# Performance work log

Measured on AMD Instinct MI355X. Metric: run time of the kernel, lower is better.

The kernel has to match this reference:

```python
import jax, jax.numpy as jnp
import numpy as np

EPS = 1e-12  # matches torch F.normalize default eps


def _l2norm(x):
    n = jnp.linalg.norm(x, axis=-1, keepdims=True)
    return x / jnp.maximum(n, EPS)


def setup_inputs() -> dict:
    key = jax.random.key(0)
    k1, k2 = jax.random.split(key)
    B, Na, T, Nv, D = 16, 128, 10, 196, 256
    audio_feats = jax.random.normal(k1, (B, Na, D), dtype=jnp.float32)
    visual_feats = jax.random.normal(k2, (B, T, Nv, D), dtype=jnp.float32)
    temperature = jnp.asarray(2.0, dtype=jnp.float32)
    return {"audio_feats": audio_feats, "visual_feats": visual_feats,
            "temperature": temperature}


def reference(audio_feats, visual_feats, temperature):
    # audio_feats: (B, Na, D); visual_feats: (B, T, Nv, D)
    a = _l2norm(audio_feats)                         # (B, Na, D)
    v = _l2norm(visual_feats)                        # (B, T, Nv, D)
    # all-pairs token-level cosine sims: (Bx, By, Na, T, Nv)
    sims = jnp.einsum('xad,ytvd->xyatv', a, v) / temperature
    # aggregate: max over patches, mean over time, mean over audio tokens
    clip_sims = sims.max(axis=-1).mean(axis=-1).mean(axis=-1)  # (B, B)

    # InfoNCE on diagonal
    B = clip_sims.shape[0]
    diag = jnp.arange(B)
    log_p_a2v = jax.nn.log_softmax(clip_sims, axis=1)
    log_p_v2a = jax.nn.log_softmax(clip_sims.T, axis=1)
    losses = -(log_p_a2v[diag, diag] + log_p_v2a[diag, diag])
    contrastive_loss = 0.5 * losses.mean()

    # regularization: non-negativity pressure + temperature band [1, 3]
    neg = jnp.minimum(sims, 0.0)
    l_nonneg = jnp.mean(neg * neg)
    log_t = jnp.log(temperature)
    temp_low = jnp.maximum(-log_t, 0.0) ** 4
    temp_high = jnp.maximum(log_t - jnp.log(3.0), 0.0) ** 4
    reg_loss = l_nonneg + temp_low + temp_high

    total_loss = contrastive_loss + 0.3 * reg_loss
    return (total_loss, contrastive_loss, reg_loss)
```

## Files before the change

### kernel.cpp

```cpp
#include <hip/hip_runtime.h>
#include <stdint.h>


typedef float f32x16 __attribute__((ext_vector_type(16)));

#define WS_A_OFF  ((size_t)0)
#define WS_V_OFF  ((size_t)(1u<<20))
#define WS_CP_OFF (WS_V_OFF + (size_t)16*2560*256)

#define NINF (-3.4e38f)

__device__ __forceinline__ int fenc(float f) {
    int i = __float_as_int(f);
    return i >= 0 ? i : (i ^ 0x7fffffff);
}
__device__ __forceinline__ float fdec(int i) {
    return __int_as_float(i >= 0 ? i : (i ^ 0x7fffffff));
}
__device__ __forceinline__ void gld_lds16(const char* g, char* l) {
    __builtin_amdgcn_global_load_lds(
        (const __attribute__((address_space(1))) void*)g,
        (__attribute__((address_space(3))) void*)l, 16, 0, 0);
}

__global__ __launch_bounds__(256) void prep_kernel(const float* __restrict__ audio,
                                                   const float* __restrict__ visual,
                                                   char* __restrict__ ws)
{
    const int wave = blockIdx.x * 4 + (threadIdx.x >> 6);
    const int lane = threadIdx.x & 63;
    const int half = lane >> 5;
    const int sub  = lane & 31;
    const int row  = wave * 2 + half;

    float f[8];
    #pragma unroll
    for (int i = 0; i < 8; ++i) f[i] = 0.f;
    size_t dst;
    if (row < 2048) {
        const float* s = audio + (size_t)row * 256 + sub * 8;
        *(float4*)(f)     = *(const float4*)(s);
        *(float4*)(f + 4) = *(const float4*)(s + 4);
        dst = WS_A_OFF + (size_t)row * 256 + sub * 8;
    } else {
        const int vr  = row - 2048;
        const int y   = vr / 2560;
        const int rem = vr - y * 2560;
        const int t   = rem >> 8;
        const int vv  = rem & 255;
        if (vv < 196) {
            const float* s = visual + (size_t)((y*10 + t)*196 + vv) * 256 + sub * 8;
            *(float4*)(f)     = *(const float4*)(s);
            *(float4*)(f + 4) = *(const float4*)(s + 4);
        }
        dst = WS_V_OFF + (size_t)vr * 256 + (size_t)((sub ^ (vr & 31)) << 3);
    }

    float ss = 0.f;
    #pragma unroll
    for (int i = 0; i < 8; ++i) ss += f[i] * f[i];
    #pragma unroll
    for (int m = 1; m < 32; m <<= 1) ss += __shfl_xor(ss, m);
    const float sc = 1.0f / fmaxf(sqrtf(ss), 1e-12f);

    int w0 = __builtin_amdgcn_cvt_pk_fp8_f32(f[0]*sc, f[1]*sc, 0, false);
    w0     = __builtin_amdgcn_cvt_pk_fp8_f32(f[2]*sc, f[3]*sc, w0, true);
    int w1 = __builtin_amdgcn_cvt_pk_fp8_f32(f[4]*sc, f[5]*sc, 0, false);
    w1     = __builtin_amdgcn_cvt_pk_fp8_f32(f[6]*sc, f[7]*sc, w1, true);
    *(uint2*)(ws + dst) = make_uint2((unsigned)w0, (unsigned)w1);
}

#define STAGE(c_, buf_) do {                                          \
    const char* s_ = vbase + (size_t)(c_) * 16384 + tid * 16;         \
    char* d_ = &smem[buf_][0] + tid * 16;                             \
    gld_lds16(s_,         d_);         gld_lds16(s_ +  4096, d_ +  4096); \
    gld_lds16(s_ +  8192, d_ +  8192); gld_lds16(s_ + 12288, d_ + 12288); \
} while (0)

__global__ __launch_bounds__(256, 4) void main_kernel(char* __restrict__ ws)
{
    __shared__ __align__(16) char smem[2][16384];
    __shared__ int part[320];
    __shared__ float red[8];

    const int tid  = threadIdx.x;
    const int lane = tid & 63;
    const int wid  = tid >> 6;
    const int aw   = wid & 1;
    const int vw   = wid >> 1;
    const int l31  = lane & 31;
    const int hi   = lane >> 5;

    const int b = blockIdx.x;
    const int xcd = b & 7, s = b >> 3;
    const int y  = xcd * 2 + (s >> 6);
    const int x2 = (s & 63) >> 1;
    const int h  = s & 1;

    for (int i = tid; i < 320; i += 256) part[i] = (int)0x80000000;

    uint64_t af[16];
    {
        const char* ab = ws + WS_A_OFF + (size_t)(x2*64 + aw*32 + l31) * 256 + hi*8;
        #pragma unroll
        for (int k = 0; k < 16; ++k)
            af[k] = *(const uint64_t*)(ab + k*16);
    }
    asm volatile("s_waitcnt vmcnt(0)" ::: "memory");
    __syncthreads();

    const char* vbase = ws + WS_V_OFF + ((size_t)y * 2560 + (size_t)h * 1280) * 256;

    float nn = 0.f, rmax = NINF;

    STAGE(0, 0);

    for (int c = 0; c < 20; ++c) {
        if (c < 19) {
            STAGE(c + 1, (c + 1) & 1);
            asm volatile("s_waitcnt vmcnt(4)" ::: "memory");
        } else {
            asm volatile("s_waitcnt vmcnt(0)" ::: "memory");
        }
        __builtin_amdgcn_s_barrier();

        const int f  = 2*c + vw;
        const int ft = f & 7;
        if (ft != 7) {
            const char* bb = &smem[c & 1][0] + (vw*32 + l31) * 256;
            uint64_t vf[16];
            #pragma unroll
            for (int k = 0; k < 16; ++k)
                vf[k] = *(const uint64_t*)(bb + (((k*2 + hi) ^ l31) << 3));

            f32x16 acc = {};
            #pragma unroll
            for (int k = 0; k < 16; ++k)
                acc = __builtin_amdgcn_mfma_f32_32x32x16_fp8_fp8(
                    (long)vf[k], (long)af[k], acc, 0, 0, 0);

            #pragma unroll
            for (int i = 0; i < 16; ++i) {
                const float g = fminf(acc[i], 0.f);
                nn = fmaf(g, g, nn);
            }
            float m;
            if (ft == 6) {
                m = fmaxf(fmaxf(acc[0], acc[1]), fmaxf(acc[2], acc[3]));
                if (hi) m = NINF;
            } else {
                float a0 = fmaxf(fmaxf(acc[0], acc[1]),   fmaxf(acc[2], acc[3]));
                float a1 = fmaxf(fmaxf(acc[4], acc[5]),   fmaxf(acc[6], acc[7]));
                float a2 = fmaxf(fmaxf(acc[8], acc[9]),   fmaxf(acc[10], acc[11]));
                float a3 = fmaxf(fmaxf(acc[12], acc[13]), fmaxf(acc[14], acc[15]));
                m = fmaxf(fmaxf(a0, a1), fmaxf(a2, a3));
            }
            rmax = fmaxf(rmax, m);
        }

        if ((c & 3) == 3) {
            const int tl = c >> 2;
            float v = fmaxf(rmax, __shfl_xor(rmax, 32));
            if (hi == 0)
                atomicMax(&part[(aw*32 + l31) * 5 + tl], fenc(v));
            rmax = NINF;
        }
        asm volatile("" ::: "memory");
        __builtin_amdgcn_s_barrier();
    }

    __syncthreads();

    float sum = 0.f;
    for (int i = tid; i < 320; i += 256) sum += fdec(part[i]);
    #pragma unroll
    for (int m = 1; m < 64; m <<= 1) {
        sum += __shfl_xor(sum, m);
        nn  += __shfl_xor(nn, m);
    }
    if (lane == 0) { red[wid] = sum; red[4 + wid] = nn; }
    __syncthreads();
    if (tid == 0) {
        float S = 0.f, N = 0.f;
        #pragma unroll
        for (int w = 0; w < 4; ++w) { S += red[w]; N += red[4 + w]; }
        float* cp = (float*)(ws + WS_CP_OFF);
        const int idx = (x2*16 + y)*2 + h;
        cp[idx]        = S;
        cp[1024 + idx] = N;
    }
}

__global__ void final_kernel(const char* __restrict__ ws,
                             const float* __restrict__ temp,
                             float* __restrict__ out)
{
    __shared__ float cs[16][17];
    __shared__ float nnred[256];
    __shared__ float lse_r[16], lse_c[16];
    const int tid = threadIdx.x;
    const float T = temp[0];
    const float* cp = (const float*)(ws + WS_CP_OFF);
    const int x = tid >> 4, yy = tid & 15;
    float sclip = 0.f;
    #pragma unroll
    for (int a = 0; a < 2; ++a)
        #pragma unroll
        for (int hh = 0; hh < 2; ++hh)
            sclip += cp[(((2*x + a)*16 + yy)*2) + hh];
    cs[x][yy] = sclip / (1280.0f * T);
    float n = 0.f;
    #pragma unroll
    for (int j = 0; j < 4; ++j) n += cp[1024 + tid + j*256];
    nnred[tid] = n;
    __syncthreads();
    for (int s = 128; s > 0; s >>= 1) {
        if (tid < s) nnred[tid] += nnred[tid + s];
        __syncthreads();
    }
    if (tid < 16) {
        float m = NINF;
        for (int j = 0; j < 16; ++j) m = fmaxf(m, cs[tid][j]);
        float s = 0.f;
        for (int j = 0; j < 16; ++j) s += expf(cs[tid][j] - m);
        lse_r[tid] = m + logf(s);
    } else if (tid < 32) {
        const int c = tid - 16;
        float m = NINF;
        for (int j = 0; j < 16; ++j) m = fmaxf(m, cs[j][c]);
        float s = 0.f;
        for (int j = 0; j < 16; ++j) s += expf(cs[j][c] - m);
        lse_c[c] = m + logf(s);
    }
    __syncthreads();
    if (tid == 0) {
        float acc = 0.f;
        for (int i = 0; i < 16; ++i)
            acc += (lse_r[i] - cs[i][i]) + (lse_c[i] - cs[i][i]);
        const float contrastive = 0.5f * acc * (1.0f / 16.0f);
        const float l_nonneg = nnred[0] / (64225280.0f * T * T);
        const float lt = logf(T);
        float tl = fmaxf(-lt, 0.f); tl = tl * tl; tl = tl * tl;
        float th = fmaxf(lt - 1.0986122886681098f, 0.f); th = th * th; th = th * th;
        const float reg = l_nonneg + tl + th;
        out[0] = contrastive + 0.3f * reg;
        out[1] = contrastive;
        out[2] = reg;
    }
}

extern "C" void kernel_launch(void* const* d_in, const int* in_sizes, int n_in,
                              void* d_out, int out_size, void* d_ws, size_t ws_size,
                              hipStream_t stream)
{
    const float* audio  = (const float*)d_in[0];
    const float* visual = (const float*)d_in[1];
    const float* temp   = (const float*)d_in[2];
    char* ws = (char*)d_ws;

    prep_kernel<<<5376, 256, 0, stream>>>(audio, visual, ws);
    main_kernel<<<1024, 256, 0, stream>>>(ws);
    final_kernel<<<1, 256, 0, stream>>>(ws, temp, (float*)d_out);
}
```

Before: 121.5 us.

## Triple-buffer visual tiles and split MFMA loop into prioritized half-phases

Moves from double to triple buffering of the LDS visual tiles, so each chunk is prefetched two iterations ahead, and lowers launch bounds from 4 to 3 blocks per CU to fit the extra buffer. Each iteration's 16 MFMAs are split into two halves of 8, with barriers and s_setprio raised around the MFMA bursts so waves interleave LDS reads with matrix work. The aim is to hide global-to-LDS latency and LDS read latency behind compute, at the cost of lower occupancy and more barriers per iteration.

Measured after the change: 135.0 us. +11.1%, slower.

```diff
diff --git a/kernel.cpp b/kernel.cpp
--- a/kernel.cpp
+++ b/kernel.cpp
@@ -77,9 +77,9 @@
     gld_lds16(s_ +  8192, d_ +  8192); gld_lds16(s_ + 12288, d_ + 12288); \
 } while (0)
 
-__global__ __launch_bounds__(256, 4) void main_kernel(char* __restrict__ ws)
-{
-    __shared__ __align__(16) char smem[2][16384];
+__global__ __launch_bounds__(256, 3) void main_kernel(char* __restrict__ ws)
+{
+    __shared__ __align__(16) char smem[3][16384];
     __shared__ int part[320];
     __shared__ float red[8];
 
@@ -107,38 +107,65 @@
             af[k] = *(const uint64_t*)(ab + k*16);
     }
     asm volatile("s_waitcnt vmcnt(0)" ::: "memory");
-    __syncthreads();
 
     const char* vbase = ws + WS_V_OFF + ((size_t)y * 2560 + (size_t)h * 1280) * 256;
 
     float nn = 0.f, rmax = NINF;
 
     STAGE(0, 0);
-
+    STAGE(1, 1);
+    asm volatile("s_waitcnt vmcnt(4) lgkmcnt(0)" ::: "memory");
+    __builtin_amdgcn_s_barrier();
+
+    int bc = 0;
     for (int c = 0; c < 20; ++c) {
-        if (c < 19) {
-            STAGE(c + 1, (c + 1) & 1);
-            asm volatile("s_waitcnt vmcnt(4)" ::: "memory");
-        } else {
-            asm volatile("s_waitcnt vmcnt(0)" ::: "memory");
-        }
-        __builtin_amdgcn_s_barrier();
+        const int bs = (bc >= 1) ? bc - 1 : 2;
+        if (c + 2 < 20) STAGE(c + 2, bs);
 
         const int f  = 2*c + vw;
         const int ft = f & 7;
-        if (ft != 7) {
-            const char* bb = &smem[c & 1][0] + (vw*32 + l31) * 256;
-            uint64_t vf[16];
-            #pragma unroll
-            for (int k = 0; k < 16; ++k)
-                vf[k] = *(const uint64_t*)(bb + (((k*2 + hi) ^ l31) << 3));
-
-            f32x16 acc = {};
-            #pragma unroll
-            for (int k = 0; k < 16; ++k)
+        const bool ok = (ft != 7);
+        const char* bb = &smem[bc][0] + (vw*32 + l31) * 256;
+
+        f32x16 acc = {};
+        uint64_t vfa[8];
+
+        if (ok) {
+            #pragma unroll
+            for (int k = 0; k < 8; ++k)
+                vfa[k] = *(const uint64_t*)(bb + (((k*2 + hi) ^ l31) << 3));
+        }
+        __builtin_amdgcn_s_barrier();
+        asm volatile("s_waitcnt lgkmcnt(0)" ::: "memory");
+        __builtin_amdgcn_sched_barrier(0);
+        __builtin_amdgcn_s_setprio(1);
+        if (ok) {
+            #pragma unroll
+            for (int k = 0; k < 8; ++k)
                 acc = __builtin_amdgcn_mfma_f32_32x32x16_fp8_fp8(
-                    (long)vf[k], (long)af[k], acc, 0, 0, 0);
-
+                    (long)vfa[k], (long)af[k], acc, 0, 0, 0);
+        }
+        __builtin_amdgcn_s_setprio(0);
+        __builtin_amdgcn_s_barrier();
+
+        if (ok) {
+            #pragma unroll
+            for (int k = 0; k < 8; ++k)
+                vfa[k] = *(const uint64_t*)(bb + ((((k + 8)*2 + hi) ^ l31) << 3));
+        }
+        __builtin_amdgcn_s_barrier();
+        asm volatile("s_waitcnt lgkmcnt(0)" ::: "memory");
+        __builtin_amdgcn_sched_barrier(0);
+        __builtin_amdgcn_s_setprio(1);
+        if (ok) {
+            #pragma unroll
+            for (int k = 0; k < 8; ++k)
+                acc = __builtin_amdgcn_mfma_f32_32x32x16_fp8_fp8(
+                    (long)vfa[k], (long)af[k + 8], acc, 0, 0, 0);
+        }
+        __builtin_amdgcn_s_setprio(0);
+
+        if (ok) {
             #pragma unroll
             for (int i = 0; i < 16; ++i) {
                 const float g = fminf(acc[i], 0.f);
@@ -157,7 +184,6 @@
             }
             rmax = fmaxf(rmax, m);
         }
-
         if ((c & 3) == 3) {
             const int tl = c >> 2;
             float v = fmaxf(rmax, __shfl_xor(rmax, 32));
@@ -165,8 +191,11 @@
                 atomicMax(&part[(aw*32 + l31) * 5 + tl], fenc(v));
             rmax = NINF;
         }
-        asm volatile("" ::: "memory");
-        __builtin_amdgcn_s_barrier();
+
+        if (c < 18) asm volatile("s_waitcnt vmcnt(4)" ::: "memory");
+        else        asm volatile("s_waitcnt vmcnt(0)" ::: "memory");
+        __builtin_amdgcn_s_barrier();
+        bc = (bc + 1 == 3) ? 0 : bc + 1;
     }
 
     __syncthreads();
```
